# Kernel tuning notes

Hardware: AMD Instinct MI355X
Metric: run time of the kernel (lower is better)

Reference implementation:

```python
import jax, jax.numpy as jnp
import numpy as np

K = 32           # number of neighbors (init kwarg k)
NUM_CLASSES = 100  # fixed class vocabulary for jit-compatible bincount


def setup_inputs() -> dict:
    key = jax.random.key(0)
    k1, k2, k3 = jax.random.split(key, 3)
    X_test = jax.random.normal(k1, (2048, 512), dtype=jnp.float32)
    X_train = jax.random.normal(k2, (65536, 512), dtype=jnp.float32)
    y_train = jax.random.randint(k3, (65536,), 0, NUM_CLASSES, dtype=jnp.int32)
    return {"X_test": X_test, "X_train": X_train, "y_train": y_train}


def reference(X_test, X_train, y_train):
    # Pairwise euclidean distances via ||q||^2 - 2 q.t + ||t||^2  -> [Nq, Nt]
    q2 = jnp.sum(X_test * X_test, axis=1, keepdims=True)        # [Nq, 1]
    t2 = jnp.sum(X_train * X_train, axis=1)                      # [Nt]
    d2 = q2 - 2.0 * (X_test @ X_train.T) + t2[None, :]           # [Nq, Nt]
    dist = jnp.sqrt(jnp.maximum(d2, 0.0))
    # k smallest distances -> neighbor indices
    _, idx = jax.lax.top_k(-dist, K)                             # [Nq, K]
    neighbor_labels = y_train[idx]                               # [Nq, K]
    # bincount per query (vectorized) + argmax = majority vote
    counts = jnp.sum(jax.nn.one_hot(neighbor_labels, NUM_CLASSES, dtype=jnp.float32), axis=1)  # [Nq, C]
    y_pred = jnp.argmax(counts, axis=1).astype(jnp.int32)        # [Nq]
    return y_pred
```

## Files before the change

kernel.cpp:

```cpp
#include <hip/hip_runtime.h>
#include <hip/hip_bf16.h>
#include <stdint.h>

typedef unsigned long long u64;
typedef unsigned int u32;
typedef unsigned short u16;
typedef __attribute__((ext_vector_type(8))) short short8;
typedef __attribute__((ext_vector_type(16))) float float16;

#define NQ 2048
#define NT 65536
#define DIM 512
#define KNN 32
#define NC 100
#define NS 32

#define QT 32
#define SLICE (NT / NS)
#define TT 256
#define KK 16
#define FCAP 32

#define PQT 32
#define PTT 256
#define PSLICE 512
#define NTPRE 2048

#define MQT 128
#define MTT 128
#define MBK 32
#define MSLICE 2048
#define SCAP 16
#define NTILES 256

#define GCAP 4096

#define GBUF 24576

__global__ void norm_kernel(const float* __restrict__ X, float* __restrict__ out, int nrows) {
    int row = blockIdx.x * 4 + (threadIdx.x >> 6);
    int lane = threadIdx.x & 63;
    if (row >= nrows) return;
    const float4* p = (const float4*)(X + (size_t)row * DIM);
    float4 a = p[lane];
    float4 b = p[lane + 64];
    float s = a.x*a.x + a.y*a.y + a.z*a.z + a.w*a.w
            + b.x*b.x + b.y*b.y + b.z*b.z + b.w*b.w;
    #pragma unroll
    for (int off = 32; off > 0; off >>= 1) s += __shfl_down(s, off, 64);
    if (lane == 0) out[row] = s;
}

__global__ void split_kernel(const float* __restrict__ X, u16* __restrict__ H,
                             u16* __restrict__ L, int n4) {
    int i = blockIdx.x * 256 + threadIdx.x;
    if (i >= n4) return;
    float4 v = ((const float4*)X)[i];
    float f[4] = {v.x, v.y, v.z, v.w};
    u16 hh[4], ll[4];
    #pragma unroll
    for (int j = 0; j < 4; ++j) {
        union { __hip_bfloat16 b; u16 u; } cv;
        cv.b = __float2bfloat16(f[j]);
        hh[j] = cv.u;
        float hf = __bfloat162float(cv.b);
        cv.b = __float2bfloat16(f[j] - hf);
        ll[j] = cv.u;
    }
    ((ushort4*)H)[i] = make_ushort4(hh[0], hh[1], hh[2], hh[3]);
    ((ushort4*)L)[i] = make_ushort4(ll[0], ll[1], ll[2], ll[3]);
}

__launch_bounds__(256, 2)
__global__ void knn_pre(const float* __restrict__ Xq, const float* __restrict__ Xt,
                        const float* __restrict__ q2, const float* __restrict__ t2,
                        float* __restrict__ Dpre) {
    __shared__ float sQ[KK][PQT];
    __shared__ float sT[KK][PTT];

    const int tid = threadIdx.x;
    const int q0 = blockIdx.x * PQT;
    const int t0p = blockIdx.y * PSLICE;
    const int tq4 = (tid >> 5) * 4;
    const int tt4 = (tid & 31) * 4;
    const int pg = tid & 63;
    const int kg = tid >> 6;
    const int qp = tid & 31;
    const int kq = tid >> 5;

    float qq[4];
    #pragma unroll
    for (int i = 0; i < 4; ++i) qq[i] = q2[q0 + tq4 + i];

    #pragma unroll 1
    for (int chunk = 0; chunk < PSLICE / PTT; ++chunk) {
        const int tbase = t0p + chunk * PTT;
        float acc[4][8];
        #pragma unroll
        for (int i = 0; i < 4; ++i)
            #pragma unroll
            for (int j = 0; j < 8; ++j) acc[i][j] = 0.f;

        #pragma unroll 1
        for (int k0 = 0; k0 < DIM; k0 += KK) {
            __syncthreads();
            {
                const float* Tp = Xt + (size_t)(tbase + pg * 4) * DIM + k0 + kg * 4;
                float4 r0 = *(const float4*)(Tp);
                float4 r1 = *(const float4*)(Tp + DIM);
                float4 r2 = *(const float4*)(Tp + 2 * DIM);
                float4 r3 = *(const float4*)(Tp + 3 * DIM);
                *(float4*)&sT[kg * 4 + 0][pg * 4] = make_float4(r0.x, r1.x, r2.x, r3.x);
                *(float4*)&sT[kg * 4 + 1][pg * 4] = make_float4(r0.y, r1.y, r2.y, r3.y);
                *(float4*)&sT[kg * 4 + 2][pg * 4] = make_float4(r0.z, r1.z, r2.z, r3.z);
                *(float4*)&sT[kg * 4 + 3][pg * 4] = make_float4(r0.w, r1.w, r2.w, r3.w);
            }
            {
                float2 v = *(const float2*)(Xq + (size_t)(q0 + qp) * DIM + k0 + kq * 2);
                sQ[kq * 2 + 0][qp] = v.x;
                sQ[kq * 2 + 1][qp] = v.y;
            }
            __syncthreads();
            #pragma unroll
            for (int k = 0; k < KK; ++k) {
                float4 qv = *(const float4*)&sQ[k][tq4];
                float4 ta = *(const float4*)&sT[k][tt4];
                float4 tb = *(const float4*)&sT[k][128 + tt4];
                float qa[4] = {qv.x, qv.y, qv.z, qv.w};
                float tv[8] = {ta.x, ta.y, ta.z, ta.w, tb.x, tb.y, tb.z, tb.w};
                #pragma unroll
                for (int i = 0; i < 4; ++i)
                    #pragma unroll
                    for (int j = 0; j < 8; ++j)
                        acc[i][j] = fmaf(qa[i], tv[j], acc[i][j]);
            }
        }

        float t2v[8];
        #pragma unroll
        for (int j = 0; j < 4; ++j) {
            t2v[j]     = t2[tbase + tt4 + j];
            t2v[4 + j] = t2[tbase + 128 + tt4 + j];
        }
        #pragma unroll
        for (int i = 0; i < 4; ++i) {
            float4 lo, hi;
            lo.x = fmaxf(qq[i] - 2.f * acc[i][0] + t2v[0], 0.f);
            lo.y = fmaxf(qq[i] - 2.f * acc[i][1] + t2v[1], 0.f);
            lo.z = fmaxf(qq[i] - 2.f * acc[i][2] + t2v[2], 0.f);
            lo.w = fmaxf(qq[i] - 2.f * acc[i][3] + t2v[3], 0.f);
            hi.x = fmaxf(qq[i] - 2.f * acc[i][4] + t2v[4], 0.f);
            hi.y = fmaxf(qq[i] - 2.f * acc[i][5] + t2v[5], 0.f);
            hi.z = fmaxf(qq[i] - 2.f * acc[i][6] + t2v[6], 0.f);
            hi.w = fmaxf(qq[i] - 2.f * acc[i][7] + t2v[7], 0.f);
            *(float4*)&Dpre[(size_t)(q0 + tq4 + i) * NTPRE + tbase + tt4] = lo;
            *(float4*)&Dpre[(size_t)(q0 + tq4 + i) * NTPRE + tbase + 128 + tt4] = hi;
        }
    }
}

__launch_bounds__(64)
__global__ void seed_topk(const float* __restrict__ Dpre, u32* __restrict__ seed) {
    __shared__ u64 ll[64][KNN + 1];
    const int q = blockIdx.x;
    const int lane = threadIdx.x;
    #pragma unroll
    for (int j = 0; j <= KNN; ++j) ll[lane][j] = ~0ULL;
    const float* src = Dpre + (size_t)q * NTPRE;
    u64 kth = ~0ULL;
    for (int i = lane; i < NTPRE; i += 64) {
        u64 key = (u64)__float_as_uint(src[i]);
        if (key < kth) {
            int p = KNN - 1;
            while (p > 0 && ll[lane][p - 1] > key) { ll[lane][p] = ll[lane][p - 1]; --p; }
            ll[lane][p] = key;
            kth = ll[lane][KNN - 1];
        }
    }
    __syncthreads();
    int ptr = 0;
    u64 cur = ll[lane][0];
    u64 m = 0;
    for (int it = 0; it < KNN; ++it) {
        m = cur;
        #pragma unroll
        for (int off = 32; off > 0; off >>= 1) {
            u64 o = __shfl_xor(m, off, 64);
            m = (o < m) ? o : m;
        }
        u64 got = __ballot(cur == m);
        int w = __ffsll(got) - 1;
        if (lane == w) { ++ptr; cur = (ptr < KNN) ? ll[lane][ptr] : ~0ULL; }
    }
    if (lane == 0) seed[q] = (u32)m;
}

__device__ __forceinline__ void gld16(const void* g, void* l) {
    __builtin_amdgcn_global_load_lds(
        (const __attribute__((address_space(1))) u32*)g,
        (__attribute__((address_space(3))) u32*)l, 16, 0, 0);
}

__launch_bounds__(512, 1)
__global__ void gemm_filter(const u16* __restrict__ Qh, const u16* __restrict__ Ql,
                            const u16* __restrict__ Th, const u16* __restrict__ Tl,
                            const float* __restrict__ q2, const float* __restrict__ t2,
                            const u32* __restrict__ seed,
                            u32* __restrict__ gcnt, u64* __restrict__ glist) {
    __shared__ __align__(16) u16 tiles[3][GBUF];
    __shared__ float sQ2L[128];
    __shared__ float sT2L[256];
    __shared__ u32 sSeed[128];

    const int tid = threadIdx.x;
    const int lane = tid & 63;
    const int wid = tid >> 6;
    const int bid = blockIdx.x + (int)(gridDim.x * blockIdx.y);
    const int wg  = ((bid & 7) << 9) + (bid >> 3);
    const int q0g = (wg & 15) * 128;
    const int tb  = (wg >> 4) * 256;
    const int m_off = (wid >> 2) * 64;
    const int n_off = (wid & 3) * 64;
    const int swz = ((lane >> 1) & 3) << 3;
    const int l4r = lane >> 2;
    const int l4c = (((lane & 3) ^ ((lane >> 3) & 3)) * 8);

    if (tid < 128) {
        sQ2L[tid] = q2[q0g + tid];
        sSeed[tid] = seed[q0g + tid] + 256u;
    }
    if (tid < 256) sT2L[tid] = t2[tb + tid];

    float16 acc[2][2];
    acc[0][0] = (float16)(0.0f); acc[0][1] = (float16)(0.0f);
    acc[1][0] = (float16)(0.0f); acc[1][1] = (float16)(0.0f);

    #define STAGE_TILE(BUF, K0)                                                         \
        do {                                                                            \
            _Pragma("unroll")                                                           \
            for (int s6 = 0; s6 < 6; ++s6) {                                            \
                const int ii = wid + s6 * 8;                                            \
                const u16* P; int rb, off;                                              \
                if (ii < 16) {                                                          \
                    P = (ii < 8) ? Qh : Ql; rb = q0g;                                   \
                    off = ((ii < 8) ? 0 : 4096) + (ii & 7) * 512;                       \
                    rb += (ii & 7) * 16;                                                \
                } else {                                                                \
                    const int jj = ii - 16;                                             \
                    P = (jj < 16) ? Th : Tl; rb = tb;                                   \
                    off = 8192 + ((jj < 16) ? 0 : 8192) + (jj & 15) * 512;              \
                    rb += (jj & 15) * 16;                                               \
                }                                                                       \
                gld16(P + (size_t)(rb + l4r) * DIM + (K0) + l4c,                        \
                      (u16*)tiles[BUF] + off);                                          \
            }                                                                           \
        } while (0)

    STAGE_TILE(0, 0);
    STAGE_TILE(1, MBK);
    __syncthreads();

    int cb = 0;
    #pragma unroll 1
    for (int t = 0; t < DIM / MBK; ++t) {
        const bool pf = (t + 2 < DIM / MBK);
        if (pf) {
            int bn = cb + 2; if (bn >= 3) bn -= 3;
            STAGE_TILE(bn, (t + 2) * MBK);
        }
        const u16* pAh = tiles[cb];
        const u16* pAl = pAh + 4096;
        const u16* pBh = pAh + 8192;
        const u16* pBl = pAh + 16384;
        __builtin_amdgcn_s_setprio(1);
        #pragma unroll
        for (int s = 0; s < 2; ++s) {
            const int kb = (s * 16 + (lane >> 5) * 8) ^ swz;
            short8 ah[2], al[2], bh[2], bl[2];
            #pragma unroll
            for (int mi = 0; mi < 2; ++mi) {
                int row = m_off + mi * 32 + (lane & 31);
                ah[mi] = *(const short8*)(const void*)&pAh[row * 32 + kb];
                al[mi] = *(const short8*)(const void*)&pAl[row * 32 + kb];
            }
            #pragma unroll
            for (int nj = 0; nj < 2; ++nj) {
                int row = n_off + nj * 32 + (lane & 31);
                bh[nj] = *(const short8*)(const void*)&pBh[row * 32 + kb];
                bl[nj] = *(const short8*)(const void*)&pBl[row * 32 + kb];
            }
            #pragma unroll
            for (int mi = 0; mi < 2; ++mi)
                #pragma unroll
                for (int nj = 0; nj < 2; ++nj) {
                    acc[mi][nj] = __builtin_amdgcn_mfma_f32_32x32x16_bf16(ah[mi], bh[nj], acc[mi][nj], 0, 0, 0);
                    acc[mi][nj] = __builtin_amdgcn_mfma_f32_32x32x16_bf16(ah[mi], bl[nj], acc[mi][nj], 0, 0, 0);
                    acc[mi][nj] = __builtin_amdgcn_mfma_f32_32x32x16_bf16(al[mi], bh[nj], acc[mi][nj], 0, 0, 0);
                }
        }
        __builtin_amdgcn_s_setprio(0);
        if (pf) asm volatile("s_waitcnt vmcnt(6)" ::: "memory");
        else    asm volatile("s_waitcnt vmcnt(0)" ::: "memory");
        __builtin_amdgcn_s_barrier();
        __builtin_amdgcn_sched_barrier(0);
        ++cb; if (cb >= 3) cb = 0;
    }
    #undef STAGE_TILE

    #pragma unroll
    for (int mi = 0; mi < 2; ++mi)
        #pragma unroll
        for (int nj = 0; nj < 2; ++nj) {
            const int tcol_l = n_off + nj * 32 + (lane & 31);
            const float t2v = sT2L[tcol_l];
            #pragma unroll
            for (int r = 0; r < 16; ++r) {
                const int qrow_l = m_off + mi * 32 + (r & 3) + 8 * (r >> 2) + 4 * (lane >> 5);
                float d = fmaxf(sQ2L[qrow_l] - 2.0f * acc[mi][nj][r] + t2v, 0.0f);
                if (__float_as_uint(d) <= sSeed[qrow_l]) {
                    const int q = q0g + qrow_l;
                    u32 pos = atomicAdd(&gcnt[q], 1u);
                    if (pos < GCAP)
                        glist[(size_t)q * GCAP + pos] =
                            ((u64)__float_as_uint(d) << 16) | (u64)(u32)(tb + tcol_l);
                }
            }
        }
}

__launch_bounds__(64)
__global__ void knn_topk(const u64* __restrict__ glist, const u32* __restrict__ gcnt,
                         const int* __restrict__ y_train, int* __restrict__ out) {
    __shared__ u64 ll[64][KNN + 1];
    __shared__ u64 fin[KNN];
    __shared__ int counts[NC];
    const int q = blockIdx.x;
    const int lane = threadIdx.x;
    #pragma unroll
    for (int j = 0; j <= KNN; ++j) ll[lane][j] = ~0ULL;
    for (int i = lane; i < NC; i += 64) counts[i] = 0;
    u32 n = gcnt[q]; if (n > GCAP) n = GCAP;
    const u64* src = glist + (size_t)q * GCAP;
    u64 kth = ~0ULL;
    for (u32 i = lane; i < n; i += 64) {
        u64 key = src[i];
        if (key < kth) {
            int p = KNN - 1;
            while (p > 0 && ll[lane][p - 1] > key) { ll[lane][p] = ll[lane][p - 1]; --p; }
            ll[lane][p] = key;
            kth = ll[lane][KNN - 1];
        }
    }
    __syncthreads();
    int ptr = 0;
    u64 cur = ll[lane][0];
    for (int it = 0; it < KNN; ++it) {
        u64 m = cur;
        #pragma unroll
        for (int off = 32; off > 0; off >>= 1) {
            u64 o = __shfl_xor(m, off, 64);
            m = (o < m) ? o : m;
        }
        u64 got = __ballot(cur == m);
        int w = __ffsll(got) - 1;
        if (lane == 0) fin[it] = m;
        if (lane == w) { ++ptr; cur = (ptr < KNN) ? ll[lane][ptr] : ~0ULL; }
    }
    __syncthreads();
    if (lane < KNN) {
        int idx = (int)(fin[lane] & 0xFFFF);
        atomicAdd(&counts[y_train[idx]], 1);
    }
    __syncthreads();
    if (lane == 0) {
        int bestc = counts[0], bestl = 0;
        for (int c = 1; c < NC; ++c)
            if (counts[c] > bestc) { bestc = counts[c]; bestl = c; }
        out[q] = bestl;
    }
}


__launch_bounds__(256, 2)
__global__ void knn_prepass(const float* __restrict__ Xq, const float* __restrict__ Xt,
                            const float* __restrict__ q2, const float* __restrict__ t2,
                            u32* __restrict__ seed) {
    __shared__ float sQ[KK][PQT];
    __shared__ float sT[KK][PTT];
    __shared__ float sD[PQT][PTT + 1];
    __shared__ u32 topk[PQT][KNN + 1];

    const int tid = threadIdx.x;
    const int q0 = blockIdx.x * PQT;
    const int t0p = blockIdx.y * PSLICE;
    const int tq4 = (tid >> 5) * 4;
    const int tt4 = (tid & 31) * 4;
    const int pg = tid & 63;
    const int kg = tid >> 6;
    const int qp = tid & 31;
    const int kq = tid >> 5;

    for (int i = tid; i < PQT * (KNN + 1); i += 256) ((u32*)topk)[i] = 0xFFFFFFFFu;
    u32 kth = 0xFFFFFFFFu;

    float qq[4];
    #pragma unroll
    for (int i = 0; i < 4; ++i) qq[i] = q2[q0 + tq4 + i];

    #pragma unroll 1
    for (int chunk = 0; chunk < PSLICE / PTT; ++chunk) {
        const int tbase = t0p + chunk * PTT;
        float acc[4][8];
        #pragma unroll
        for (int i = 0; i < 4; ++i)
            #pragma unroll
            for (int j = 0; j < 8; ++j) acc[i][j] = 0.f;

        #pragma unroll 1
        for (int k0 = 0; k0 < DIM; k0 += KK) {
            __syncthreads();
            {
                const float* Tp = Xt + (size_t)(tbase + pg * 4) * DIM + k0 + kg * 4;
                float4 r0 = *(const float4*)(Tp);
                float4 r1 = *(const float4*)(Tp + DIM);
                float4 r2 = *(const float4*)(Tp + 2 * DIM);
                float4 r3 = *(const float4*)(Tp + 3 * DIM);
                *(float4*)&sT[kg * 4 + 0][pg * 4] = make_float4(r0.x, r1.x, r2.x, r3.x);
                *(float4*)&sT[kg * 4 + 1][pg * 4] = make_float4(r0.y, r1.y, r2.y, r3.y);
                *(float4*)&sT[kg * 4 + 2][pg * 4] = make_float4(r0.z, r1.z, r2.z, r3.z);
                *(float4*)&sT[kg * 4 + 3][pg * 4] = make_float4(r0.w, r1.w, r2.w, r3.w);
            }
            {
                float2 v = *(const float2*)(Xq + (size_t)(q0 + qp) * DIM + k0 + kq * 2);
                sQ[kq * 2 + 0][qp] = v.x;
                sQ[kq * 2 + 1][qp] = v.y;
            }
            __syncthreads();
            #pragma unroll
            for (int k = 0; k < KK; ++k) {
                float4 qv = *(const float4*)&sQ[k][tq4];
                float4 ta = *(const float4*)&sT[k][tt4];
                float4 tb = *(const float4*)&sT[k][128 + tt4];
                float qa[4] = {qv.x, qv.y, qv.z, qv.w};
                float tv[8] = {ta.x, ta.y, ta.z, ta.w, tb.x, tb.y, tb.z, tb.w};
                #pragma unroll
                for (int i = 0; i < 4; ++i)
                    #pragma unroll
                    for (int j = 0; j < 8; ++j)
                        acc[i][j] = fmaf(qa[i], tv[j], acc[i][j]);
            }
        }

        #pragma unroll
        for (int i = 0; i < 4; ++i)
            #pragma unroll
            for (int j = 0; j < 8; ++j) {
                int t = (j < 4) ? (tt4 + j) : (128 + tt4 + (j - 4));
                sD[tq4 + i][t] = fmaxf((qq[i] - 2.f * acc[i][j]) + t2[tbase + t], 0.f);
            }
        __syncthreads();

        if (tid < PQT) {
            for (int t = 0; t < PTT; ++t) {
                u32 d = __float_as_uint(sD[tid][t]);
                if (d < kth) {
                    int p = KNN - 1;
                    while (p > 0 && topk[tid][p - 1] > d) {
                        topk[tid][p] = topk[tid][p - 1];
                        --p;
                    }
                    topk[tid][p] = d;
                    kth = topk[tid][KNN - 1];
                }
            }
        }
    }
    if (tid < PQT) atomicMin(&seed[q0 + tid], kth);
}

__device__ __forceinline__ void stage_tile(const u16* __restrict__ Qh, const u16* __restrict__ Ql,
                                           const u16* __restrict__ Th, const u16* __restrict__ Tl,
                                           u16* base, int q0, int tb, int k0, int wid, int lane) {
    const int l4r = lane >> 2;
    const int l4c = (((lane & 3) ^ ((lane >> 3) & 3)) * 8);
    #pragma unroll
    for (int u = 0; u < 4; ++u) {
        const u16* P = (u == 0) ? Qh : (u == 1) ? Ql : (u == 2) ? Th : Tl;
        const int r0 = (u < 2) ? q0 : tb;
        const u16* g = P + (size_t)(r0 + wid * 16 + l4r) * DIM + k0 + l4c;
        gld16(g, base + u * 4096 + wid * 512);
    }
}

__launch_bounds__(512, 1)
__global__ void knn_mfma(const u16* __restrict__ Qh, const u16* __restrict__ Ql,
                         const u16* __restrict__ Th, const u16* __restrict__ Tl,
                         const float* __restrict__ q2, const float* __restrict__ t2,
                         const u32* __restrict__ seed, u64* __restrict__ cand) {
    __shared__ __align__(16) u16 tiles[3][16384];
    __shared__ u32 topkD[MQT][KNN + 1];
    __shared__ u16 topkI[MQT][KNN + 1];
    __shared__ u64 sbuf[MQT][SCAP];
    __shared__ u64 kth64[MQT];
    __shared__ u32 cnt[MQT];
    __shared__ float sQ2[MQT];
    __shared__ float sT2[MTT];
    __shared__ int againF;

    const int tid = threadIdx.x;
    const int lane = tid & 63;
    const int wid = tid >> 6;
    const int q0 = blockIdx.y * MQT;
    const int s0 = blockIdx.x * MSLICE;
    const int m_off = (wid >> 2) * 64;
    const int n_off = (wid & 3) * 32;
    const int swz = ((lane >> 1) & 3) << 3;

    for (int i = tid; i < MQT * (KNN + 1); i += 512) {
        ((u32*)topkD)[i] = 0xFFFFFFFFu;
        ((u16*)topkI)[i] = 0xFFFFu;
    }
    u64 seedkey = ~0ULL;
    if (tid < MQT) {
        seedkey = ((u64)seed[q0 + tid] + 1) << 16;
        kth64[tid] = seedkey;
        cnt[tid] = 0u;
        sQ2[tid] = q2[q0 + tid];
    }
    if (tid == 0) againF = 0;

    stage_tile(Qh, Ql, Th, Tl, tiles[0], q0, s0, 0, wid, lane);
    stage_tile(Qh, Ql, Th, Tl, tiles[1], q0, s0, MBK, wid, lane);
    __syncthreads();

    int cb = 0;
    #pragma unroll 1
    for (int chunk = 0; chunk < MSLICE / MTT; ++chunk) {
        const int tb = s0 + chunk * MTT;
        float16 acc[2];
        acc[0] = (float16)(0.0f);
        acc[1] = (float16)(0.0f);

        #pragma unroll 1
        for (int t = 0; t < DIM / MBK; ++t) {
            const int Tn = chunk * 16 + t + 2;
            const bool pf = (Tn < NTILES);
            if (pf) {
                int bn = cb + 2; if (bn >= 3) bn -= 3;
                stage_tile(Qh, Ql, Th, Tl, tiles[bn], q0,
                           s0 + (Tn >> 4) * MTT, (Tn & 15) * MBK, wid, lane);
            }
            const u16* sAh = tiles[cb];
            const u16* sAl = sAh + 4096;
            const u16* sBh = sAh + 8192;
            const u16* sBl = sAh + 12288;
            #pragma unroll
            for (int s = 0; s < 2; ++s) {
                const int kb = (s * 16 + (lane >> 5) * 8) ^ swz;
                short8 ah[2], al[2];
                #pragma unroll
                for (int mi = 0; mi < 2; ++mi) {
                    int row = m_off + mi * 32 + (lane & 31);
                    ah[mi] = *(const short8*)(const void*)&sAh[row * MBK + kb];
                    al[mi] = *(const short8*)(const void*)&sAl[row * MBK + kb];
                }
                int brow = n_off + (lane & 31);
                short8 bh = *(const short8*)(const void*)&sBh[brow * MBK + kb];
                short8 bl = *(const short8*)(const void*)&sBl[brow * MBK + kb];
                #pragma unroll
                for (int mi = 0; mi < 2; ++mi) {
                    acc[mi] = __builtin_amdgcn_mfma_f32_32x32x16_bf16(ah[mi], bh, acc[mi], 0, 0, 0);
                    acc[mi] = __builtin_amdgcn_mfma_f32_32x32x16_bf16(ah[mi], bl, acc[mi], 0, 0, 0);
                    acc[mi] = __builtin_amdgcn_mfma_f32_32x32x16_bf16(al[mi], bh, acc[mi], 0, 0, 0);
                }
            }
            if (pf) asm volatile("s_waitcnt vmcnt(4)" ::: "memory");
            else    asm volatile("s_waitcnt vmcnt(0)" ::: "memory");
            __builtin_amdgcn_s_barrier();
            __builtin_amdgcn_sched_barrier(0);
            ++cb; if (cb >= 3) cb = 0;
        }

        if (tid < MTT) sT2[tid] = t2[tb + tid];
        __syncthreads();
        const float t2r = sT2[n_off + (lane & 31)];
        const int tcol = n_off + (lane & 31);

        u32 mask = 0;
        for (;;) {
            #pragma unroll
            for (int mi = 0; mi < 2; ++mi) {
                #pragma unroll
                for (int r = 0; r < 16; ++r) {
                    const int bit = mi * 16 + r;
                    if ((mask >> bit) & 1) continue;
                    const int qrow = m_off + mi * 32 + (r & 3) + 8 * (r >> 2) + 4 * (lane >> 5);
                    float d = fmaxf(sQ2[qrow] - 2.0f * acc[mi][r] + t2r, 0.0f);
                    u64 key = ((u64)__float_as_uint(d) << 16) | (u64)(u32)(tb + tcol);
                    if (key < kth64[qrow]) {
                        u32 pos = atomicAdd(&cnt[qrow], 1u);
                        if (pos < SCAP) { sbuf[qrow][pos] = key; mask |= (1u << bit); }
                    }
                }
            }
            __syncthreads();
            if (tid < MQT) {
                u32 n = cnt[tid];
                u32 m = n < SCAP ? n : SCAP;
                for (u32 e = 0; e < m; ++e) {
                    u64 key = sbuf[tid][e];
                    u64 last = ((u64)topkD[tid][KNN - 1] << 16) | topkI[tid][KNN - 1];
                    if (key < last) {
                        int p = KNN - 1;
                        while (p > 0) {
                            u64 prev = ((u64)topkD[tid][p - 1] << 16) | topkI[tid][p - 1];
                            if (prev > key) {
                                topkD[tid][p] = topkD[tid][p - 1];
                                topkI[tid][p] = topkI[tid][p - 1];
                                --p;
                            } else break;
                        }
                        topkD[tid][p] = (u32)(key >> 16);
                        topkI[tid][p] = (u16)(key & 0xFFFF);
                    }
                }
                u64 last = ((u64)topkD[tid][KNN - 1] << 16) | topkI[tid][KNN - 1];
                kth64[tid] = last < seedkey ? last : seedkey;
                if (n > SCAP) againF = 1;
                cnt[tid] = 0u;
            }
            __syncthreads();
            int go = againF;
            __syncthreads();
            if (tid == 0) againF = 0;
            if (!go) break;
            __syncthreads();
        }
    }

    __syncthreads();
    for (int i = tid; i < MQT * KNN; i += 512) {
        int q = i >> 5, k = i & 31;
        u64 key = ((u64)topkD[q][k] << 16) | topkI[q][k];
        cand[((size_t)(q0 + q) * NS + blockIdx.x) * KNN + k] = key;
    }
}

__launch_bounds__(256, 4)
__global__ void knn_part(const float* __restrict__ Xq, const float* __restrict__ Xt,
                         const float* __restrict__ q2, const float* __restrict__ t2,
                         u64* __restrict__ cand) {
    __shared__ float sQ[KK][QT];
    __shared__ float sT[KK][TT];
    __shared__ u64 topk[QT][KNN];
    __shared__ u64 buf[QT][FCAP];
    __shared__ u64 kth64[QT];
    __shared__ u32 cnt[QT];
    __shared__ int againF;

    const int tid = threadIdx.x;
    const int q0 = blockIdx.x * QT;
    const int t0 = blockIdx.y * SLICE;
    const int tq4 = (tid >> 5) * 4;
    const int tt4 = (tid & 31) * 4;
    const int pg = tid & 63;
    const int kg = tid >> 6;
    const int qp = tid & 31;
    const int kq = tid >> 5;

    for (int i = tid; i < QT * KNN; i += 256) ((u64*)topk)[i] = ~0ULL;
    if (tid < QT) { kth64[tid] = ~0ULL; cnt[tid] = 0u; }
    if (tid == 0) againF = 0;

    float qq[4];
    #pragma unroll
    for (int i = 0; i < 4; ++i) qq[i] = q2[q0 + tq4 + i];

    #pragma unroll 1
    for (int chunk = 0; chunk < SLICE / TT; ++chunk) {
        const int tbase = t0 + chunk * TT;
        float acc[4][8];
        #pragma unroll
        for (int i = 0; i < 4; ++i)
            #pragma unroll
            for (int j = 0; j < 8; ++j) acc[i][j] = 0.f;

        #pragma unroll 1
        for (int k0 = 0; k0 < DIM; k0 += KK) {
            __syncthreads();
            {
                const float* Tp = Xt + (size_t)(tbase + pg * 4) * DIM + k0 + kg * 4;
                float4 r0 = *(const float4*)(Tp);
                float4 r1 = *(const float4*)(Tp + DIM);
                float4 r2 = *(const float4*)(Tp + 2 * DIM);
                float4 r3 = *(const float4*)(Tp + 3 * DIM);
                *(float4*)&sT[kg * 4 + 0][pg * 4] = make_float4(r0.x, r1.x, r2.x, r3.x);
                *(float4*)&sT[kg * 4 + 1][pg * 4] = make_float4(r0.y, r1.y, r2.y, r3.y);
                *(float4*)&sT[kg * 4 + 2][pg * 4] = make_float4(r0.z, r1.z, r2.z, r3.z);
                *(float4*)&sT[kg * 4 + 3][pg * 4] = make_float4(r0.w, r1.w, r2.w, r3.w);
            }
            {
                float2 v = *(const float2*)(Xq + (size_t)(q0 + qp) * DIM + k0 + kq * 2);
                sQ[kq * 2 + 0][qp] = v.x;
                sQ[kq * 2 + 1][qp] = v.y;
            }
            __syncthreads();
            #pragma unroll
            for (int k = 0; k < KK; ++k) {
                float4 qv = *(const float4*)&sQ[k][tq4];
                float4 ta = *(const float4*)&sT[k][tt4];
                float4 tb = *(const float4*)&sT[k][128 + tt4];
                float qa[4] = {qv.x, qv.y, qv.z, qv.w};
                float tv[8] = {ta.x, ta.y, ta.z, ta.w, tb.x, tb.y, tb.z, tb.w};
                #pragma unroll
                for (int i = 0; i < 4; ++i)
                    #pragma unroll
                    for (int j = 0; j < 8; ++j)
                        acc[i][j] = fmaf(qa[i], tv[j], acc[i][j]);
            }
        }

        float t2v[8];
        #pragma unroll
        for (int j = 0; j < 4; ++j) {
            t2v[j]     = t2[tbase + tt4 + j];
            t2v[4 + j] = t2[tbase + 128 + tt4 + j];
        }
        #pragma unroll
        for (int i = 0; i < 4; ++i)
            #pragma unroll
            for (int j = 0; j < 8; ++j)
                acc[i][j] = fmaxf((qq[i] - 2.f * acc[i][j]) + t2v[j], 0.f);

        unsigned mask = 0;
        for (;;) {
            u64 kv[4];
            #pragma unroll
            for (int i = 0; i < 4; ++i) kv[i] = kth64[tq4 + i];
            #pragma unroll
            for (int i = 0; i < 4; ++i) {
                #pragma unroll
                for (int j = 0; j < 8; ++j) {
                    unsigned b = 1u << (i * 8 + j);
                    if (mask & b) continue;
                    int tloc = (j < 4) ? (tt4 + j) : (128 + tt4 + (j - 4));
                    u64 key = ((u64)__float_as_uint(acc[i][j]) << 16) |
                              (u64)(unsigned)(tbase + tloc);
                    if (key < kv[i]) {
                        unsigned pos = atomicAdd(&cnt[tq4 + i], 1u);
                        if (pos < FCAP) { buf[tq4 + i][pos] = key; mask |= b; }
                    }
                }
            }
            __syncthreads();
            if (tid < QT) {
                unsigned n = cnt[tid];
                unsigned m = n < FCAP ? n : FCAP;
                for (unsigned e = 0; e < m; ++e) {
                    u64 key = buf[tid][e];
                    if (key < topk[tid][KNN - 1]) {
                        int p = KNN - 1;
                        while (p > 0 && topk[tid][p - 1] > key) {
                            topk[tid][p] = topk[tid][p - 1];
                            --p;
                        }
                        topk[tid][p] = key;
                    }
                }
                kth64[tid] = topk[tid][KNN - 1];
                if (n > FCAP) againF = 1;
                cnt[tid] = 0u;
            }
            __syncthreads();
            int go = againF;
            __syncthreads();
            if (tid == 0) againF = 0;
            if (!go) break;
            __syncthreads();
        }
    }

    __syncthreads();
    for (int i = tid; i < QT * KNN; i += 256) {
        int q = i >> 5, k = i & 31;
        cand[((size_t)(q0 + q) * NS + blockIdx.y) * KNN + k] = topk[q][k];
    }
}

__global__ void knn_merge(const u64* __restrict__ cand,
                          const int* __restrict__ y_train, int* __restrict__ out) {
    __shared__ u64 keys[NS * KNN];
    __shared__ u64 top[KNN];
    __shared__ int counts[NC];
    int q = blockIdx.x;
    for (int i = threadIdx.x; i < NS * KNN; i += 64)
        keys[i] = cand[(size_t)q * NS * KNN + i];
    for (int i = threadIdx.x; i < NC; i += 64) counts[i] = 0;
    if (threadIdx.x < KNN) top[threadIdx.x] = ~0ULL;
    __syncthreads();

    if (threadIdx.x == 0) {
        for (int s = 0; s < NS; ++s) {
            for (int j = 0; j < KNN; ++j) {
                u64 key = keys[s * KNN + j];
                if (key >= top[KNN - 1]) break;
                int p = KNN - 1;
                while (p > 0 && top[p - 1] > key) { top[p] = top[p - 1]; --p; }
                top[p] = key;
            }
        }
        for (int k = 0; k < KNN; ++k) {
            int idx = (int)(top[k] & 0xFFFF);
            counts[y_train[idx]]++;
        }
        int bestc = counts[0], bestl = 0;
        for (int c = 1; c < NC; ++c)
            if (counts[c] > bestc) { bestc = counts[c]; bestl = c; }
        out[q] = bestl;
    }
}

extern "C" void kernel_launch(void* const* d_in, const int* in_sizes, int n_in,
                              void* d_out, int out_size, void* d_ws, size_t ws_size,
                              hipStream_t stream) {
    const float* Xq = (const float*)d_in[0];
    const float* Xt = (const float*)d_in[1];
    const int*   y  = (const int*)d_in[2];
    int* out = (int*)d_out;

    float* t2 = (float*)d_ws;
    float* q2 = t2 + NT;
    u64* cand = (u64*)(q2 + NQ);
    u32* seed = (u32*)(cand + (size_t)NQ * NS * KNN);
    u16* Qh = (u16*)(seed + NQ);
    u16* Ql = Qh + (size_t)NQ * DIM;
    u16* Th = Ql + (size_t)NQ * DIM;
    u16* Tl = Th + (size_t)NT * DIM;
    u64* glist = (u64*)(Tl + (size_t)NT * DIM);
    u32* gcnt  = (u32*)(glist + (size_t)NQ * GCAP);
    float* Dpre = (float*)glist;

    const size_t need = (size_t)(NT + NQ) * 4
                      + (size_t)NQ * NS * KNN * 8
                      + (size_t)NQ * 4
                      + 2 * ((size_t)NQ * DIM + (size_t)NT * DIM) * 2;
    const bool use_mfma = ws_size >= need;
    const bool use_filter = ws_size >= need + (size_t)NQ * GCAP * 8 + (size_t)NQ * 4;

    norm_kernel<<<NT / 4, 256, 0, stream>>>(Xt, t2, NT);
    norm_kernel<<<NQ / 4, 256, 0, stream>>>(Xq, q2, NQ);
    if (use_mfma && use_filter) {
        split_kernel<<<(NQ * DIM / 4 + 255) / 256, 256, 0, stream>>>(Xq, Qh, Ql, NQ * DIM / 4);
        split_kernel<<<(NT * DIM / 4 + 255) / 256, 256, 0, stream>>>(Xt, Th, Tl, NT * DIM / 4);
        knn_pre<<<dim3(NQ / PQT, NTPRE / PSLICE), 256, 0, stream>>>(Xq, Xt, q2, t2, Dpre);
        seed_topk<<<NQ, 64, 0, stream>>>(Dpre, seed);
        hipMemsetAsync(gcnt, 0, NQ * sizeof(u32), stream);
        gemm_filter<<<dim3(NQ / 128, NT / 256), 512, 0, stream>>>(
            Qh, Ql, Th, Tl, q2, t2, seed, gcnt, glist);
        knn_topk<<<NQ, 64, 0, stream>>>(glist, gcnt, y, out);
    } else if (use_mfma) {
        hipMemsetAsync(seed, 0xFF, NQ * sizeof(u32), stream);
        split_kernel<<<(NQ * DIM / 4 + 255) / 256, 256, 0, stream>>>(Xq, Qh, Ql, NQ * DIM / 4);
        split_kernel<<<(NT * DIM / 4 + 255) / 256, 256, 0, stream>>>(Xt, Th, Tl, NT * DIM / 4);
        knn_prepass<<<dim3(NQ / PQT, NTPRE / PSLICE), 256, 0, stream>>>(Xq, Xt, q2, t2, seed);
        knn_mfma<<<dim3(NT / MSLICE, NQ / MQT), 512, 0, stream>>>(Qh, Ql, Th, Tl, q2, t2, seed, cand);
        knn_merge<<<NQ, 64, 0, stream>>>(cand, y, out);
    } else {
        knn_part<<<dim3(NQ / QT, NS), 256, 0, stream>>>(Xq, Xt, q2, t2, cand);
        knn_merge<<<NQ, 64, 0, stream>>>(cand, y, out);
    }
}
```

Before: 1.230 ms.

## Enlarge gemm_filter tile to 256x256 with double-buffered LDS staging

The filtering GEMM now processes a 256-query by 256-train tile per workgroup instead of 128x256, with each wave computing a 64x128 sub-tile (2x4 MFMA accumulators). This raises arithmetic intensity and halves redundant train-tile loads from global memory. To fit LDS, the triple-buffered pipeline becomes double-buffered with one tile prefetched ahead and a full vmcnt(0) wait each step, which reduces how much load latency can be hidden. The extra accumulators also raise register pressure.

```diff
diff --git a/kernel.cpp b/kernel.cpp
--- a/kernel.cpp
+++ b/kernel.cpp
@@ -35,7 +35,7 @@
 
 #define GCAP 4096
 
-#define GBUF 24576
+#define G2BUF 32768
 
 __global__ void norm_kernel(const float* __restrict__ X, float* __restrict__ out, int nrows) {
     int row = blockIdx.x * 4 + (threadIdx.x >> 6);
@@ -207,76 +207,68 @@
                             const float* __restrict__ q2, const float* __restrict__ t2,
                             const u32* __restrict__ seed,
                             u32* __restrict__ gcnt, u64* __restrict__ glist) {
-    __shared__ __align__(16) u16 tiles[3][GBUF];
-    __shared__ float sQ2L[128];
+    __shared__ __align__(16) u16 tiles[2][G2BUF];
+    __shared__ float sQ2L[256];
     __shared__ float sT2L[256];
-    __shared__ u32 sSeed[128];
+    __shared__ u32 sSeed[256];
 
     const int tid = threadIdx.x;
     const int lane = tid & 63;
     const int wid = tid >> 6;
     const int bid = blockIdx.x + (int)(gridDim.x * blockIdx.y);
-    const int wg  = ((bid & 7) << 9) + (bid >> 3);
-    const int q0g = (wg & 15) * 128;
-    const int tb  = (wg >> 4) * 256;
-    const int m_off = (wid >> 2) * 64;
-    const int n_off = (wid & 3) * 64;
+    const int wg  = ((bid & 7) << 8) + (bid >> 3);
+    const int q0g = (wg & 7) * 256;
+    const int tb  = (wg >> 3) * 256;
+    const int m_off = (wid >> 1) * 64;
+    const int n_off = (wid & 1) * 128;
     const int swz = ((lane >> 1) & 3) << 3;
     const int l4r = lane >> 2;
     const int l4c = (((lane & 3) ^ ((lane >> 3) & 3)) * 8);
 
-    if (tid < 128) {
+    if (tid < 256) {
         sQ2L[tid] = q2[q0g + tid];
         sSeed[tid] = seed[q0g + tid] + 256u;
-    }
-    if (tid < 256) sT2L[tid] = t2[tb + tid];
-
-    float16 acc[2][2];
-    acc[0][0] = (float16)(0.0f); acc[0][1] = (float16)(0.0f);
-    acc[1][0] = (float16)(0.0f); acc[1][1] = (float16)(0.0f);
+        sT2L[tid] = t2[tb + tid];
+    }
+
+    float16 acc[2][4];
+    #pragma unroll
+    for (int mi = 0; mi < 2; ++mi)
+        #pragma unroll
+        for (int nj = 0; nj < 4; ++nj) acc[mi][nj] = (float16)(0.0f);
 
     #define STAGE_TILE(BUF, K0)                                                         \
         do {                                                                            \
             _Pragma("unroll")                                                           \
-            for (int s6 = 0; s6 < 6; ++s6) {                                            \
-                const int ii = wid + s6 * 8;                                            \
+            for (int s8 = 0; s8 < 8; ++s8) {                                            \
+                const int ii = wid + s8 * 8;                                            \
                 const u16* P; int rb, off;                                              \
-                if (ii < 16) {                                                          \
-                    P = (ii < 8) ? Qh : Ql; rb = q0g;                                   \
-                    off = ((ii < 8) ? 0 : 4096) + (ii & 7) * 512;                       \
-                    rb += (ii & 7) * 16;                                                \
-                } else {                                                                \
-                    const int jj = ii - 16;                                             \
-                    P = (jj < 16) ? Th : Tl; rb = tb;                                   \
-                    off = 8192 + ((jj < 16) ? 0 : 8192) + (jj & 15) * 512;              \
-                    rb += (jj & 15) * 16;                                               \
-                }                                                                       \
+                if (ii < 16)      { P = Qh; rb = q0g + ii * 16;        off = ii * 512; }          \
+                else if (ii < 32) { P = Ql; rb = q0g + (ii - 16) * 16; off = 8192 + (ii - 16) * 512; } \
+                else if (ii < 48) { P = Th; rb = tb + (ii - 32) * 16;  off = 16384 + (ii - 32) * 512; } \
+                else              { P = Tl; rb = tb + (ii - 48) * 16;  off = 24576 + (ii - 48) * 512; } \
                 gld16(P + (size_t)(rb + l4r) * DIM + (K0) + l4c,                        \
                       (u16*)tiles[BUF] + off);                                          \
             }                                                                           \
         } while (0)
 
     STAGE_TILE(0, 0);
-    STAGE_TILE(1, MBK);
     __syncthreads();
 
-    int cb = 0;
+    int cur = 0;
     #pragma unroll 1
     for (int t = 0; t < DIM / MBK; ++t) {
-        const bool pf = (t + 2 < DIM / MBK);
-        if (pf) {
-            int bn = cb + 2; if (bn >= 3) bn -= 3;
-            STAGE_TILE(bn, (t + 2) * MBK);
-        }
-        const u16* pAh = tiles[cb];
-        const u16* pAl = pAh + 4096;
-        const u16* pBh = pAh + 8192;
-        const u16* pBl = pAh + 16384;
+        if (t + 1 < DIM / MBK) STAGE_TILE(cur ^ 1, (t + 1) * MBK);
+
+        const u16* pAh = tiles[cur];
+        const u16* pAl = pAh + 8192;
+        const u16* pBh = pAh + 16384;
+        const u16* pBl = pAh + 24576;
         __builtin_amdgcn_s_setprio(1);
         #pragma unroll
         for (int s = 0; s < 2; ++s) {
             const int kb = (s * 16 + (lane >> 5) * 8) ^ swz;
-            short8 ah[2], al[2], bh[2], bl[2];
+            short8 ah[2], al[2], bh[4], bl[4];
             #pragma unroll
             for (int mi = 0; mi < 2; ++mi) {
                 int row = m_off + mi * 32 + (lane & 31);
@@ -284,7 +276,7 @@
                 al[mi] = *(const short8*)(const void*)&pAl[row * 32 + kb];
             }
             #pragma unroll
-            for (int nj = 0; nj < 2; ++nj) {
+            for (int nj = 0; nj < 4; ++nj) {
                 int row = n_off + nj * 32 + (lane & 31);
                 bh[nj] = *(const short8*)(const void*)&pBh[row * 32 + kb];
                 bl[nj] = *(const short8*)(const void*)&pBl[row * 32 + kb];
@@ -292,25 +284,24 @@
             #pragma unroll
             for (int mi = 0; mi < 2; ++mi)
                 #pragma unroll
-                for (int nj = 0; nj < 2; ++nj) {
+                for (int nj = 0; nj < 4; ++nj) {
                     acc[mi][nj] = __builtin_amdgcn_mfma_f32_32x32x16_bf16(ah[mi], bh[nj], acc[mi][nj], 0, 0, 0);
                     acc[mi][nj] = __builtin_amdgcn_mfma_f32_32x32x16_bf16(ah[mi], bl[nj], acc[mi][nj], 0, 0, 0);
                     acc[mi][nj] = __builtin_amdgcn_mfma_f32_32x32x16_bf16(al[mi], bh[nj], acc[mi][nj], 0, 0, 0);
                 }
         }
         __builtin_amdgcn_s_setprio(0);
-        if (pf) asm volatile("s_waitcnt vmcnt(6)" ::: "memory");
-        else    asm volatile("s_waitcnt vmcnt(0)" ::: "memory");
+        asm volatile("s_waitcnt vmcnt(0)" ::: "memory");
         __builtin_amdgcn_s_barrier();
         __builtin_amdgcn_sched_barrier(0);
-        ++cb; if (cb >= 3) cb = 0;
+        cur ^= 1;
     }
     #undef STAGE_TILE
 
     #pragma unroll
     for (int mi = 0; mi < 2; ++mi)
         #pragma unroll
-        for (int nj = 0; nj < 2; ++nj) {
+        for (int nj = 0; nj < 4; ++nj) {
             const int tcol_l = n_off + nj * 32 + (lane & 31);
             const float t2v = sT2L[tcol_l];
             #pragma unroll
@@ -855,7 +846,7 @@
         knn_pre<<<dim3(NQ / PQT, NTPRE / PSLICE), 256, 0, stream>>>(Xq, Xt, q2, t2, Dpre);
         seed_topk<<<NQ, 64, 0, stream>>>(Dpre, seed);
         hipMemsetAsync(gcnt, 0, NQ * sizeof(u32), stream);
-        gemm_filter<<<dim3(NQ / 128, NT / 256), 512, 0, stream>>>(
+        gemm_filter<<<dim3(NQ / 256, NT / 256), 512, 0, stream>>>(
             Qh, Ql, Th, Tl, q2, t2, seed, gcnt, glist);
         knn_topk<<<NQ, 64, 0, stream>>>(glist, gcnt, y, out);
     } else if (use_mfma) {
```

Result: faster. 1.103 ms (-10.3%).
